# Kernel optimization log

Measured on AMD Instinct MI355X. Metric: run time of the kernel, lower is better.

The kernel has to match this reference:

```python
import jax, jax.numpy as jnp
import numpy as np

TEMPERATURE = 0.07
BASE_TEMPERATURE = 0.07
EPS = 1e-12


def setup_inputs() -> dict:
    key = jax.random.key(0)
    features = jax.random.normal(key, (4096, 2, 128), dtype=jnp.float32)
    return {"features": features}


def reference(features):
    bsz, n_views, d = features.shape
    n = bsz * n_views
    # torch.cat(torch.unbind(features, dim=1), dim=0): view-major stacking -> [N, D]
    cf = jnp.swapaxes(features, 0, 1).reshape(n, d)
    # L2-normalize rows
    cf = cf / jnp.linalg.norm(cf, axis=-1, keepdims=True)
    # Pairwise L2 distance via Gram matrix: ||a-b||^2 = 2 - 2 a.b for unit vectors.
    # Equivalent math to (cf[:,None]-cf).norm(dim=-1) without the (N,N,D) intermediate.
    gram = cf @ cf.T  # [N, N]
    dist = jnp.sqrt(jnp.clip(2.0 - 2.0 * gram, EPS))
    anchor_dot_contrast = 1.0 - dist  # [N, N]
    logits_max = jax.lax.stop_gradient(jnp.max(anchor_dot_contrast, axis=1, keepdims=True))
    logits = anchor_dot_contrast - logits_max
    # positives mask: same original sample, different row/col in tiled layout
    mask = jnp.tile(jnp.eye(bsz, dtype=jnp.float32), (n_views, n_views))  # [N, N]
    logits_mask = 1.0 - jnp.eye(n, dtype=jnp.float32)  # exclude self
    mask = mask * logits_mask
    exp_logits = jnp.exp(logits) * logits_mask
    log_prob = logits - jnp.log(jnp.sum(exp_logits, axis=1, keepdims=True))
    mean_log_prob_pos = jnp.sum(mask * log_prob, axis=1) / jnp.sum(mask, axis=1)
    loss = -(TEMPERATURE / BASE_TEMPERATURE) * mean_log_prob_pos
    return jnp.mean(loss.reshape(n_views, bsz))
```

## Files before the change

### kernel.cpp

```cpp
#include <hip/hip_runtime.h>
#include <math.h>

#define BSZ   4096
#define NROWS 8192
#define DIM   128
#define EPSC  1e-12f
#define NRB   64
#define NTILES 2080

typedef _Float16 half8 __attribute__((ext_vector_type(8)));
typedef float    f32x4 __attribute__((ext_vector_type(4)));

typedef __attribute__((address_space(1))) const unsigned int gas_u32;
typedef __attribute__((address_space(3))) unsigned int       las_u32;

__device__ __forceinline__ void stageB(_Float16* lds, const char* gsrc, int w, int lane) {
    #pragma unroll
    for (int it = 0; it < 8; ++it) {
        int c = w * 8 + it;
        __builtin_amdgcn_global_load_lds(
            (gas_u32*)(gsrc + c * 1024 + lane * 16),
            (las_u32*)((char*)lds + c * 1024), 16, 0, 0);
    }
}

__global__ __launch_bounds__(256) void norm_zero_kernel(
    const float* __restrict__ feat, float* __restrict__ cf,
    unsigned int* __restrict__ hsw, float* __restrict__ s, float* __restrict__ out)
{
    int t = blockIdx.x * 256 + threadIdx.x;
    if (t < NROWS) s[t] = 0.0f;
    if (t == 0) out[0] = 0.0f;

    int row  = t >> 6;
    int lane = t & 63;
    int v = row >> 12;
    int b = row & 4095;
    const float* src = feat + (size_t)b * 256 + (size_t)v * 128;
    float2 x = *(const float2*)(src + lane * 2);
    float ss = x.x * x.x + x.y * x.y;
    #pragma unroll
    for (int m = 32; m >= 1; m >>= 1) ss += __shfl_xor(ss, m, 64);
    float inv = 1.0f / sqrtf(ss);
    float2 o; o.x = x.x * inv; o.y = x.y * inv;
    *(float2*)(cf + (size_t)row * DIM + lane * 2) = o;

    union { _Float16 h[2]; unsigned int u; } cv;
    cv.h[0] = (_Float16)o.x;
    cv.h[1] = (_Float16)o.y;
    size_t off = (size_t)row * 256 + ((lane * 4) ^ ((row & 7) << 4));
    *(unsigned int*)((char*)hsw + off) = cv.u;
}

__global__ __launch_bounds__(256, 2) void gram_tri_kernel(
    const _Float16* __restrict__ h, float* __restrict__ s)
{
    __shared__ _Float16 bt[128 * 128];

    int t    = threadIdx.x;
    int w    = t >> 6;
    int lane = t & 63;
    int r16  = lane & 15;
    int g    = lane >> 4;
    int wr   = w >> 1, wc = w & 1;
    int swz  = (r16 & 7) << 4;
    const char* hb = (const char*)h;

    int bid = blockIdx.x;
    int rb = (int)(64.5f - sqrtf(64.5f * 64.5f - 2.0f * (float)bid));
    rb = rb < 0 ? 0 : (rb > 63 ? 63 : rb);
    while (rb > 0 && 64 * rb - (rb * (rb - 1)) / 2 > bid) --rb;
    while (rb < 63 && 64 * (rb + 1) - ((rb + 1) * rb) / 2 <= bid) ++rb;
    int cb = rb + (bid - (64 * rb - (rb * (rb - 1)) / 2));
    int i0 = rb * 128, j0 = cb * 128;

    half8 A[4][4];
    #pragma unroll
    for (int f = 0; f < 4; ++f) {
        size_t rowoff = (size_t)(i0 + wr * 64 + f * 16 + r16) * 256;
        #pragma unroll
        for (int ks = 0; ks < 4; ++ks)
            A[f][ks] = *(const half8*)(hb + rowoff + ((ks * 64 + g * 16) ^ swz));
    }
    stageB(bt, hb + (size_t)j0 * 256, w, lane);
    asm volatile("s_waitcnt vmcnt(0)" ::: "memory");
    __builtin_amdgcn_s_barrier();

    f32x4 acc[4][4];
    #pragma unroll
    for (int fr = 0; fr < 4; ++fr)
        #pragma unroll
        for (int fc = 0; fc < 4; ++fc) acc[fr][fc] = (f32x4){0.f, 0.f, 0.f, 0.f};

    const char* bb = (const char*)bt;
    #pragma unroll
    for (int ks = 0; ks < 4; ++ks) {
        half8 B[4];
        #pragma unroll
        for (int fc = 0; fc < 4; ++fc)
            B[fc] = *(const half8*)(bb + (wc * 64 + fc * 16 + r16) * 256
                                       + ((ks * 64 + g * 16) ^ swz));
        #pragma unroll
        for (int fr = 0; fr < 4; ++fr)
            #pragma unroll
            for (int fc = 0; fc < 4; ++fc)
                acc[fr][fc] = __builtin_amdgcn_mfma_f32_16x16x32_f16(
                    A[fr][ks], B[fc], acc[fr][fc], 0, 0, 0);
    }

    int dw = (rb == cb) && (wr == wc);
    int eq[4];
    #pragma unroll
    for (int q = 0; q < 4; ++q) eq[q] = (g * 4 + q) == r16;

    float rs[4][4], rc[4] = {0.f, 0.f, 0.f, 0.f};
    #pragma unroll
    for (int fr = 0; fr < 4; ++fr)
        #pragma unroll
        for (int q = 0; q < 4; ++q) rs[fr][q] = 0.0f;

    #pragma unroll
    for (int fr = 0; fr < 4; ++fr)
        #pragma unroll
        for (int fc = 0; fc < 4; ++fc)
            #pragma unroll
            for (int q = 0; q < 4; ++q) {
                float gv = acc[fr][fc][q];
                float t2 = fmaxf(fmaf(-2.0f, gv, 2.0f), EPSC);
                float e  = __expf(-__builtin_amdgcn_sqrtf(t2));
                if (dw && (fr == fc) && eq[q]) e = 0.0f;
                rs[fr][q] += e;
                rc[fc]    += e;
            }

    #pragma unroll
    for (int fr = 0; fr < 4; ++fr)
        #pragma unroll
        for (int q = 0; q < 4; ++q) {
            float v = rs[fr][q];
            v += __shfl_xor(v, 1, 64);
            v += __shfl_xor(v, 2, 64);
            v += __shfl_xor(v, 4, 64);
            v += __shfl_xor(v, 8, 64);
            if (r16 == 0)
                atomicAdd(&s[i0 + wr * 64 + fr * 16 + g * 4 + q], v);
        }

    if (rb != cb) {
        #pragma unroll
        for (int fc = 0; fc < 4; ++fc) {
            float v = rc[fc];
            v += __shfl_xor(v, 16, 64);
            v += __shfl_xor(v, 32, 64);
            if (g == 0)
                atomicAdd(&s[j0 + wc * 64 + fc * 16 + r16], v);
        }
    }
}

__global__ __launch_bounds__(1024) void finish_kernel(
    const float* __restrict__ cf, const float* __restrict__ s,
    float* __restrict__ out)
{
    __shared__ float red[16];
    int w    = threadIdx.x >> 6;
    int lane = threadIdx.x & 63;
    int i = blockIdx.x * 16 + w;
    int p = (i + BSZ) & (NROWS - 1);
    float2 x = *(const float2*)(cf + (size_t)i * DIM + lane * 2);
    float2 y = *(const float2*)(cf + (size_t)p * DIM + lane * 2);
    float d = x.x * y.x + x.y * y.y;
    #pragma unroll
    for (int m = 32; m >= 1; m >>= 1) d += __shfl_xor(d, m, 64);
    if (lane == 0) {
        float t2  = fmaxf(2.0f - 2.0f * d, EPSC);
        float adc = 1.0f - sqrtf(t2);
        red[w] = 1.0f + logf(s[i]) - adc;
    }
    __syncthreads();
    if (threadIdx.x == 0) {
        float acc = 0.f;
        #pragma unroll
        for (int k = 0; k < 16; ++k) acc += red[k];
        atomicAdd(out, acc * (1.0f / NROWS));
    }
}

extern "C" void kernel_launch(void* const* d_in, const int* in_sizes, int n_in,
                              void* d_out, int out_size, void* d_ws, size_t ws_size,
                              hipStream_t stream)
{
    const float* feat = (const float*)d_in[0];
    float* out = (float*)d_out;
    float* cf  = (float*)d_ws;
    float* s   = cf + (size_t)NROWS * DIM;
    unsigned int* hsw = (unsigned int*)(s + NROWS);

    norm_zero_kernel<<<(NROWS * 64) / 256, 256, 0, stream>>>(feat, cf, hsw, s, out);
    gram_tri_kernel<<<NTILES, 256, 0, stream>>>((const _Float16*)hsw, s);
    finish_kernel<<<NROWS / 16, 1024, 0, stream>>>(cf, s, out);
}
```

Measured before the change: 102.0 us.

## Fuse finish pass into gram kernel via per-row-block completion counters

Removes the separate finish kernel launch. Each gram tile increments per-row-block counters, and the block that completes a row block computes the positive-pair term and log of the row sums for its 128 rows. A global done counter lets the last finalizer write the mean. This trades a kernel launch and its tail for extra atomics and serialized tail work inside a few gram blocks, each of which finalizes 128 rows with 4 waves.

```diff
diff --git a/kernel.cpp b/kernel.cpp
--- a/kernel.cpp
+++ b/kernel.cpp
@@ -26,11 +26,12 @@
 
 __global__ __launch_bounds__(256) void norm_zero_kernel(
     const float* __restrict__ feat, float* __restrict__ cf,
-    unsigned int* __restrict__ hsw, float* __restrict__ s, float* __restrict__ out)
+    unsigned int* __restrict__ hsw, float* __restrict__ s,
+    unsigned int* __restrict__ aux)
 {
     int t = blockIdx.x * 256 + threadIdx.x;
     if (t < NROWS) s[t] = 0.0f;
-    if (t == 0) out[0] = 0.0f;
+    if (t < 66) aux[t] = 0u;
 
     int row  = t >> 6;
     int lane = t & 63;
@@ -52,10 +53,56 @@
     *(unsigned int*)((char*)hsw + off) = cv.u;
 }
 
+__device__ void finalize_rows(const float* __restrict__ cf,
+                              const float* __restrict__ s,
+                              float* outsum, unsigned int* donecnt,
+                              float* out, int R0, int t)
+{
+    __shared__ float red[4];
+    int w = t >> 6, lane = t & 63;
+    float acc = 0.0f;
+    for (int rr = 0; rr < 32; ++rr) {
+        int i = R0 + w * 32 + rr;
+        int p = (i + BSZ) & (NROWS - 1);
+        float2 x = *(const float2*)(cf + (size_t)i * DIM + lane * 2);
+        float2 y = *(const float2*)(cf + (size_t)p * DIM + lane * 2);
+        float d = x.x * y.x + x.y * y.y;
+        #pragma unroll
+        for (int m = 32; m >= 1; m >>= 1) d += __shfl_xor(d, m, 64);
+        if (lane == 0) {
+            float si = __hip_atomic_load(&s[i], __ATOMIC_RELAXED,
+                                         __HIP_MEMORY_SCOPE_AGENT);
+            float t2  = fmaxf(2.0f - 2.0f * d, EPSC);
+            acc += 1.0f + logf(si) - (1.0f - sqrtf(t2));
+        }
+    }
+    if (lane == 0) red[w] = acc;
+    __syncthreads();
+    if (t == 0) {
+        float b = red[0] + red[1] + red[2] + red[3];
+        atomicAdd(outsum, b);
+        __threadfence();
+        unsigned int old = atomicAdd(donecnt, 1u);
+        if (old == NRB - 1) {
+            float tot = __hip_atomic_load(outsum, __ATOMIC_RELAXED,
+                                          __HIP_MEMORY_SCOPE_AGENT);
+            out[0] = tot * (1.0f / (float)NROWS);
+        }
+    }
+    __syncthreads();
+}
+
 __global__ __launch_bounds__(256, 2) void gram_tri_kernel(
-    const _Float16* __restrict__ h, float* __restrict__ s)
+    const _Float16* __restrict__ h, const float* __restrict__ cf,
+    float* __restrict__ s, unsigned int* __restrict__ aux,
+    float* __restrict__ out)
 {
     __shared__ _Float16 bt[128 * 128];
+    __shared__ int fl[2];
+
+    unsigned int* blkcnt  = aux;
+    float*        outsum  = (float*)(aux + 64);
+    unsigned int* donecnt = aux + 65;
 
     int t    = threadIdx.x;
     int w    = t >> 6;
@@ -156,34 +203,18 @@
                 atomicAdd(&s[j0 + wc * 64 + fc * 16 + r16], v);
         }
     }
-}
-
-__global__ __launch_bounds__(1024) void finish_kernel(
-    const float* __restrict__ cf, const float* __restrict__ s,
-    float* __restrict__ out)
-{
-    __shared__ float red[16];
-    int w    = threadIdx.x >> 6;
-    int lane = threadIdx.x & 63;
-    int i = blockIdx.x * 16 + w;
-    int p = (i + BSZ) & (NROWS - 1);
-    float2 x = *(const float2*)(cf + (size_t)i * DIM + lane * 2);
-    float2 y = *(const float2*)(cf + (size_t)p * DIM + lane * 2);
-    float d = x.x * y.x + x.y * y.y;
-    #pragma unroll
-    for (int m = 32; m >= 1; m >>= 1) d += __shfl_xor(d, m, 64);
-    if (lane == 0) {
-        float t2  = fmaxf(2.0f - 2.0f * d, EPSC);
-        float adc = 1.0f - sqrtf(t2);
-        red[w] = 1.0f + logf(s[i]) - adc;
-    }
-    __syncthreads();
-    if (threadIdx.x == 0) {
-        float acc = 0.f;
-        #pragma unroll
-        for (int k = 0; k < 16; ++k) acc += red[k];
-        atomicAdd(out, acc * (1.0f / NROWS));
-    }
+
+    __syncthreads();
+    if (t == 0) {
+        __threadfence();
+        int ro = atomicAdd(&blkcnt[rb], 1u);
+        int co = (rb != cb) ? (int)atomicAdd(&blkcnt[cb], 1u) : -1;
+        fl[0] = ro; fl[1] = co;
+    }
+    __syncthreads();
+    int ro = fl[0], co = fl[1];
+    if (ro == NRB - 1) finalize_rows(cf, s, outsum, donecnt, out, i0, t);
+    if (co == NRB - 1) finalize_rows(cf, s, outsum, donecnt, out, j0, t);
 }
 
 extern "C" void kernel_launch(void* const* d_in, const int* in_sizes, int n_in,
@@ -195,8 +226,8 @@
     float* cf  = (float*)d_ws;
     float* s   = cf + (size_t)NROWS * DIM;
     unsigned int* hsw = (unsigned int*)(s + NROWS);
-
-    norm_zero_kernel<<<(NROWS * 64) / 256, 256, 0, stream>>>(feat, cf, hsw, s, out);
-    gram_tri_kernel<<<NTILES, 256, 0, stream>>>((const _Float16*)hsw, s);
-    finish_kernel<<<NROWS / 16, 1024, 0, stream>>>(cf, s, out);
-}
+    unsigned int* aux = hsw + (size_t)NROWS * DIM / 2;
+
+    norm_zero_kernel<<<(NROWS * 64) / 256, 256, 0, stream>>>(feat, cf, hsw, s, aux);
+    gram_tri_kernel<<<NTILES, 256, 0, stream>>>((const _Float16*)hsw, cf, s, aux, out);
+}
```

After: 180.9 us. 77.3% more time.
